# Optimization experiments

Measured on AMD Instinct MI355X. Metric: run time of the kernel, lower is better.

## Reference

```python
import jax, jax.numpy as jnp
import numpy as np

B, T, C = 4, 2048, 1024


def setup_inputs() -> dict:
    key = jax.random.key(0)
    ks = jax.random.split(key, 5)
    s = 1.0 / np.sqrt(C)
    return {
        "X": jax.random.normal(ks[0], (B, T, C), dtype=jnp.float32),
        "Wq": jax.random.normal(ks[1], (C, C), dtype=jnp.float32) * s,
        "Wk": jax.random.normal(ks[2], (C, C), dtype=jnp.float32) * s,
        "Wv": jax.random.normal(ks[3], (C, C), dtype=jnp.float32) * s,
        "Wo": jax.random.normal(ks[4], (C, C), dtype=jnp.float32) * s,
    }


def reference(X, Wq, Wk, Wv, Wo):
    Bx, Tx, Cx = X.shape
    Q = X @ Wq  # [B,T,C]
    K = X @ Wk
    V = X @ Wv
    scores = jnp.einsum('btc,bsc->bts', Q, K) / jnp.sqrt(jnp.asarray(Cx, X.dtype))
    # causal mask: position t attends to s <= t
    causal = jnp.tril(jnp.ones((Tx, Tx), dtype=bool))
    scores = jnp.where(causal, scores, jnp.asarray(-jnp.inf, scores.dtype))
    weights = jax.nn.softmax(scores, axis=-1)
    out = jnp.einsum('bts,bsc->btc', weights, V)
    return out @ Wo
```

## Files before the change

kernel.cpp:

```cpp
#include <hip/hip_runtime.h>
#include <hip/hip_bf16.h>
#include <cmath>


typedef __attribute__((ext_vector_type(8))) __bf16 bf16x8;
typedef __attribute__((ext_vector_type(8))) short short8;
typedef __attribute__((ext_vector_type(4))) float f32x4;

__device__ __forceinline__ unsigned short f2bf(float f) {
  union { float f; unsigned u; } v; v.f = f;
  unsigned u = v.u;
  u += ((u >> 16) & 1u) + 0x7fffu;
  return (unsigned short)(u >> 16);
}
__device__ __forceinline__ float bf2f(unsigned short h) {
  union { unsigned u; float f; } v; v.u = ((unsigned)h) << 16;
  return v.f;
}

#define GLDS(gp, sp)                                                           \
  __builtin_amdgcn_global_load_lds(                                            \
      (const __attribute__((address_space(1))) void*)(gp),                     \
      (__attribute__((address_space(3))) void*)(sp), 16, 0, 0)

__global__ void prep(const float* __restrict__ X,
                     const float* __restrict__ w0, const float* __restrict__ w1,
                     const float* __restrict__ w2, const float* __restrict__ w3,
                     unsigned short* __restrict__ Xb,
                     unsigned short* __restrict__ wcat,
                     unsigned short* __restrict__ wvb,
                     unsigned short* __restrict__ wot,
                     int n) {
  if (blockIdx.z == 2) {
    int bx = blockIdx.x * 32, by = blockIdx.y * 32;
    int tx = threadIdx.x, ty = threadIdx.y;
#pragma unroll
    for (int i = 0; i < 32; i += 8) {
      size_t idx = (size_t)(by + ty + i) * n + bx + tx;
      wvb[idx] = f2bf(w2[idx]);
    }
  } else if (blockIdx.z < 4) {
    const float* src = blockIdx.z == 0 ? w0 : blockIdx.z == 1 ? w1 : w3;
    unsigned short* dst = blockIdx.z == 0 ? wcat
                          : blockIdx.z == 1 ? wcat + (size_t)n * n : wot;
    __shared__ float tile[32][33];
    int bx = blockIdx.x * 32, by = blockIdx.y * 32;
    int tx = threadIdx.x, ty = threadIdx.y;
#pragma unroll
    for (int i = 0; i < 32; i += 8)
      tile[ty + i][tx] = src[(size_t)(by + ty + i) * n + bx + tx];
    __syncthreads();
#pragma unroll
    for (int i = 0; i < 32; i += 8)
      dst[(size_t)(bx + ty + i) * n + by + tx] = f2bf(tile[tx][ty + i]);
  } else {
    const int bid = (blockIdx.z - 4) * 1024 + blockIdx.y * 32 + blockIdx.x;
    const int t = threadIdx.y * 32 + threadIdx.x;
    const int i = (bid * 256 + t) * 4;
    float4 f = *(const float4*)(X + i);
    ushort4 o = make_ushort4(f2bf(f.x), f2bf(f.y), f2bf(f.z), f2bf(f.w));
    *(ushort4*)(Xb + i) = o;
  }
}

template <typename OutT, int NW>
__global__ __launch_bounds__(NW * 64, NW / 2)
void gemm_bt(const unsigned short* __restrict__ A, int lda, long long sA,
             const unsigned short* __restrict__ B, int ldb, long long sB,
             OutT* __restrict__ Cp, int ldc, long long sC,
             int K, float alpha, int tri, int kcap, int gx) {
  A  += (long long)blockIdx.z * sA;
  B  += (long long)blockIdx.z * sB;
  Cp += (long long)blockIdx.z * sC;

  int by, bx;
  if (tri) {
    const int idx = blockIdx.x;
    by = (int)((sqrtf(8.f * idx + 1.f) - 1.f) * 0.5f);
    while (by * (by + 1) / 2 > idx) --by;
    while ((by + 1) * (by + 2) / 2 <= idx) ++by;
    bx = idx - by * (by + 1) / 2;
  } else if (gx > 0) {
    const int id = blockIdx.x;
    const int gs = gx * 8;
    const int g = id / gs, r = id - g * gs;
    bx = r >> 3;
    by = g * 8 + (r & 7);
    if (kcap) by = (gridDim.x / gx) - 1 - by;
  } else {
    by = blockIdx.y;
    bx = blockIdx.x;
  }
  const int m0 = by * 128;
  const int n0 = bx * 128;
  const int Keff = kcap ? min(K, m0 + 128) : K;

  const int tid  = threadIdx.x;
  const int lane = tid & 63;
  const int w    = tid >> 6;
  const int wm   = (NW == 4) ? (w >> 1) * 64 : (w >> 1) * 32;
  const int wn   = (w & 1) * 64;
  const int quad = lane >> 4;
  const int l16  = lane & 15;
  constexpr int AI = (NW == 4) ? 4 : 2;
  constexpr int NR = 128 / (NW * 8);

  __shared__ unsigned short As[8192];
  __shared__ unsigned short Bs[8192];

  f32x4 acc[AI][4];
#pragma unroll
  for (int i = 0; i < AI; ++i)
#pragma unroll
    for (int j = 0; j < 4; ++j)
      acc[i][j] = (f32x4){0.f, 0.f, 0.f, 0.f};

  const int srow = tid >> 3;
  const int scol = ((tid & 7) ^ (srow & 7)) * 8;
  const unsigned short* gA = A + (long long)(m0 + srow) * lda + scol;
  const unsigned short* gB = B + (long long)(n0 + srow) * ldb + scol;
  const int rsw = l16 & 7;

  for (int kt = 0; kt < Keff; kt += 64) {
    __syncthreads();
#pragma unroll
    for (int r = 0; r < NR; ++r) {
      GLDS(gA + (long long)(r * NW * 8) * lda + kt, As + r * NW * 512 + tid * 8);
      GLDS(gB + (long long)(r * NW * 8) * ldb + kt, Bs + r * NW * 512 + tid * 8);
    }
    __syncthreads();
#pragma unroll
    for (int ks = 0; ks < 2; ++ks) {
      bf16x8 af[AI], bfr[4];
#pragma unroll
      for (int i = 0; i < AI; ++i)
        af[i] = *(const bf16x8*)(As + (wm + i * 16 + l16) * 64 +
                                 ((ks * 4 + quad) ^ rsw) * 8);
#pragma unroll
      for (int j = 0; j < 4; ++j)
        bfr[j] = *(const bf16x8*)(Bs + (wn + j * 16 + l16) * 64 +
                                  ((ks * 4 + quad) ^ rsw) * 8);
#pragma unroll
      for (int i = 0; i < AI; ++i)
#pragma unroll
        for (int j = 0; j < 4; ++j)
          acc[i][j] = __builtin_amdgcn_mfma_f32_16x16x32_bf16(af[i], bfr[j],
                                                              acc[i][j], 0, 0, 0);
    }
  }

#pragma unroll
  for (int i = 0; i < AI; ++i) {
#pragma unroll
    for (int j = 0; j < 4; ++j) {
      const int row = m0 + wm + i * 16 + quad * 4;
      const int col = n0 + wn + j * 16 + l16;
#pragma unroll
      for (int r = 0; r < 4; ++r) {
        float v = acc[i][j][r] * alpha;
        if constexpr (sizeof(OutT) == 2)
          Cp[(long long)(row + r) * ldc + col] = (OutT)f2bf(v);
        else
          Cp[(long long)(row + r) * ldc + col] = v;
      }
    }
  }
}


#define STG(tt, st, bb) do {                                                  \
    const int ld_ = (st) < 2 ? lda : ldb;                                     \
    const unsigned short* gp_ = ((st) < 2 ? gA : gB)                          \
        + (long long)(((st) & 1) * 128) * ld_ + (long long)(tt) * 64;         \
    unsigned short* sp_ = smem + ((bb) << 15) + (((st) >= 2) ? 16384 : 0)     \
        + (((st) & 1) * 128) * 64 + tid * 8;                                  \
    GLDS(gp_, sp_);                                                           \
    GLDS(gp_ + (long long)64 * ld_, sp_ + 4096);                              \
  } while (0)

#define LDA_PH(mh)                                                            \
  _Pragma("unroll") for (int i = 0; i < 4; ++i)                               \
  _Pragma("unroll") for (int ks = 0; ks < 2; ++ks)                            \
    bA[i][ks] = *(const bf16x8*)(Ab + (wm + (mh) * 64 + i * 16 + l16) * 64 +  \
                                 (((ks * 4 + quad) ^ rsw) * 8));

#define LDB_PH(j0)                                                            \
  _Pragma("unroll") for (int j = 0; j < 2; ++j)                               \
  _Pragma("unroll") for (int ks = 0; ks < 2; ++ks)                            \
    bB[(j0) + j][ks] = *(const bf16x8*)(Bb + (wn + ((j0) + j) * 16 + l16) * 64\
                                        + (((ks * 4 + quad) ^ rsw) * 8));

#define MM(mh, j0)                                                            \
  _Pragma("unroll") for (int i = 0; i < 4; ++i)                               \
  _Pragma("unroll") for (int j = 0; j < 2; ++j)                               \
  _Pragma("unroll") for (int ks = 0; ks < 2; ++ks)                            \
    acc[(mh) * 4 + i][(j0) + j] = __builtin_amdgcn_mfma_f32_16x16x32_bf16(    \
        bA[i][ks], bB[(j0) + j][ks], acc[(mh) * 4 + i][(j0) + j], 0, 0, 0);

#define PHASE_SYNC()                                                          \
  __builtin_amdgcn_s_barrier();                                               \
  asm volatile("s_waitcnt lgkmcnt(0)" ::: "memory");                          \
  __builtin_amdgcn_sched_barrier(0);

#define GROUP(T_, B_) do {                                                    \
    const unsigned short* Ab = smem + ((B_) << 15);                           \
    const unsigned short* Bb = Ab + 16384;                                    \
                                                                      \
    LDA_PH(0); LDB_PH(0);                                                     \
    if ((T_) + 1 < nt) STG((T_) + 1, 1, (B_) ^ 1);                            \
    asm volatile("s_waitcnt lgkmcnt(8)" ::: "memory");                        \
    PHASE_SYNC();                                                             \
    __builtin_amdgcn_s_setprio(1); MM(0, 0); __builtin_amdgcn_s_setprio(0);   \
    __builtin_amdgcn_s_barrier();                                             \
                                                                      \
    LDB_PH(2);                                                                \
    if ((T_) + 1 < nt) STG((T_) + 1, 2, (B_) ^ 1);                            \
    PHASE_SYNC();                                                             \
    __builtin_amdgcn_s_setprio(1); MM(0, 2); __builtin_amdgcn_s_setprio(0);   \
    __builtin_amdgcn_s_barrier();                                             \
                                                                      \
    LDA_PH(1);                                                                \
    if ((T_) + 1 < nt) STG((T_) + 1, 3, (B_) ^ 1);                            \
    PHASE_SYNC();                                                             \
    __builtin_amdgcn_s_setprio(1); MM(1, 2); __builtin_amdgcn_s_setprio(0);   \
    __builtin_amdgcn_s_barrier();                                             \
                                                                      \
    if ((T_) + 2 < nt) {                                                      \
      STG((T_) + 2, 0, (B_));                                                 \
      asm volatile("s_waitcnt vmcnt(2)" ::: "memory");                        \
    } else {                                                                  \
      asm volatile("s_waitcnt vmcnt(0)" ::: "memory");                        \
    }                                                                         \
    __builtin_amdgcn_s_barrier();                                             \
    __builtin_amdgcn_s_setprio(1); MM(1, 0); __builtin_amdgcn_s_setprio(0);   \
    __builtin_amdgcn_s_barrier();                                             \
  } while (0)

__global__ __launch_bounds__(512, 2)
void gemm_qkv8(const unsigned short* __restrict__ A, int lda,
               const unsigned short* __restrict__ B, int ldb,
               unsigned short* __restrict__ Cp, int K) {
  const int id  = blockIdx.x;
  const int cpx = gridDim.x >> 3;
  const int sw  = (id & 7) * cpx + (id >> 3);
  const int bx  = sw % 12;
  const int by  = sw / 12;
  const int m0  = by * 256;
  const int n0  = bx * 256;

  const int tid  = threadIdx.x;
  const int lane = tid & 63;
  const int w    = tid >> 6;
  const int wm   = (w >> 2) * 128;
  const int wn   = (w & 3) * 64;
  const int quad = lane >> 4;
  const int l16  = lane & 15;
  const int rsw  = l16 & 7;

  extern __shared__ unsigned short smem[];

  const int srow = tid >> 3;
  const int scol = ((tid & 7) ^ (srow & 7)) * 8;
  const unsigned short* gA = A + (long long)(m0 + srow) * lda + scol;
  const unsigned short* gB = B + (long long)(n0 + srow) * ldb + scol;

  f32x4 acc[8][4];
#pragma unroll
  for (int i = 0; i < 8; ++i)
#pragma unroll
    for (int j = 0; j < 4; ++j)
      acc[i][j] = (f32x4){0.f, 0.f, 0.f, 0.f};

  bf16x8 bA[4][2], bB[4][2];
  const int nt = K >> 6;

  STG(0, 0, 0); STG(0, 1, 0); STG(0, 2, 0); STG(0, 3, 0);
  STG(1, 0, 1);
  asm volatile("s_waitcnt vmcnt(2)" ::: "memory");
  __builtin_amdgcn_s_barrier();

  for (int tt = 0; tt < nt; tt += 2) {
    GROUP(tt, 0);
    GROUP(tt + 1, 1);
  }

#pragma unroll
  for (int i = 0; i < 8; ++i) {
#pragma unroll
    for (int j = 0; j < 4; ++j) {
      const int row = m0 + wm + i * 16 + quad * 4;
      const int col = n0 + wn + j * 16 + l16;
      if (col >= 2048) {
        const int b = row >> 11, t = row & 2047, cv = col - 2048;
        ushort4 o = make_ushort4(f2bf(acc[i][j][0]), f2bf(acc[i][j][1]),
                                 f2bf(acc[i][j][2]), f2bf(acc[i][j][3]));
        *(ushort4*)(Cp + 16777216LL + ((long long)(b * 1024 + cv)) * 2048 + t) = o;
      } else {
        unsigned short* dst = Cp + (col >= 1024 ? 8388608LL - 1024 : 0);
#pragma unroll
        for (int r2 = 0; r2 < 4; ++r2)
          dst[(long long)(row + r2) * 1024 + col] = f2bf(acc[i][j][r2]);
      }
    }
  }
}

#undef GROUP
#undef PHASE_SYNC
#undef MM
#undef LDB_PH
#undef LDA_PH
#undef STG

__global__ __launch_bounds__(256)
void softmax_causal(const unsigned short* __restrict__ Sin,
                    unsigned short* __restrict__ Sout, int T) {
  const long long row = blockIdx.x;
  const int t = (int)(row & (long long)(T - 1));
  const int limit = ((t >> 7) + 1) << 7;
  const unsigned short* pin = Sin + row * T;
  unsigned short* pout = Sout + row * T;
  const int tid  = threadIdx.x;
  const int base = tid * 8;
  const bool active = base < limit;

  short8 raw = {};
  if (active) raw = *(const short8*)(pin + base);
  float x[8];
  float mx = -1e30f;
#pragma unroll
  for (int j = 0; j < 8; ++j) {
    bool valid = active && (base + j) <= t;
    x[j] = valid ? bf2f((unsigned short)raw[j]) : -1e30f;
    mx = fmaxf(mx, x[j]);
  }
#pragma unroll
  for (int off = 32; off > 0; off >>= 1) mx = fmaxf(mx, __shfl_xor(mx, off));
  __shared__ float red[8];
  const int wv = tid >> 6;
  if ((tid & 63) == 0) red[wv] = mx;
  __syncthreads();
  mx = fmaxf(fmaxf(red[0], red[1]), fmaxf(red[2], red[3]));

  float sum = 0.f;
#pragma unroll
  for (int j = 0; j < 8; ++j) {
    bool valid = active && (base + j) <= t;
    x[j] = valid ? __expf(x[j] - mx) : 0.f;
    sum += x[j];
  }
#pragma unroll
  for (int off = 32; off > 0; off >>= 1) sum += __shfl_xor(sum, off);
  if ((tid & 63) == 0) red[4 + wv] = sum;
  __syncthreads();
  sum = red[4] + red[5] + red[6] + red[7];
  const float inv = 1.f / sum;

  if (active) {
    unsigned short out[8];
#pragma unroll
    for (int j = 0; j < 8; ++j) out[j] = f2bf(x[j] * inv);
    *(short8*)(pout + base) = *(const short8*)out;
  }
}

extern "C" void kernel_launch(void* const* d_in, const int* in_sizes, int n_in,
                              void* d_out, int out_size, void* d_ws,
                              size_t ws_size, hipStream_t stream) {
  (void)in_sizes; (void)n_in; (void)out_size; (void)ws_size;
  const int Bb = 4, T = 2048, C = 1024;
  const int M = Bb * T;

  const float* X  = (const float*)d_in[0];
  const float* Wq = (const float*)d_in[1];
  const float* Wk = (const float*)d_in[2];
  const float* Wv = (const float*)d_in[3];
  const float* Wo = (const float*)d_in[4];

  char* w = (char*)d_ws;
  unsigned short* Wcat = (unsigned short*)w; w += (size_t)3 * C * C * 2;
  unsigned short* Q    = (unsigned short*)w; w += (size_t)M * C * 2;
  unsigned short* Kb   = (unsigned short*)w; w += (size_t)M * C * 2;
  unsigned short* Vt   = (unsigned short*)w; w += (size_t)M * C * 2;
  unsigned short* Xb   = (unsigned short*)w; w += (size_t)M * C * 2;
  (void)Kb;
  unsigned short* Wvb  = (unsigned short*)d_out;
  unsigned short* Wot  = (unsigned short*)d_out + (size_t)C * C;
  unsigned short* S    = (unsigned short*)d_out;
  unsigned short* Sn   = Q;

  static int smem_set = 0;
  if (!smem_set) {
    hipFuncSetAttribute(reinterpret_cast<const void*>(gemm_qkv8),
                        hipFuncAttributeMaxDynamicSharedMemorySize, 131072);
    smem_set = 1;
  }

  prep<<<dim3(32, 32, 12), dim3(32, 8), 0, stream>>>(X, Wq, Wk, Wv, Wo, Xb,
                                                     Wcat, Wvb, Wot, C);

  gemm_bt<unsigned short, 4><<<dim3(C / 128, C / 128, 1), dim3(256), 0, stream>>>(
      Wot, C, 0, Wvb, C, 0, Wcat + (size_t)2 * C * C, C, 0, C, 1.f, 0, 0, 0);

  gemm_qkv8<<<dim3((M / 256) * (3 * C / 256)), dim3(512), 131072, stream>>>(
      Xb, C, Wcat, C, Q, C);

  const int ntri = (T / 128) * (T / 128 + 1) / 2;
  gemm_bt<unsigned short, 8><<<dim3(ntri, 1, Bb), dim3(512), 0, stream>>>(
      Q, C, (long long)T * C, Kb, C, (long long)T * C,
      S, T, (long long)T * T, C, 0.03125f, 1, 0, 0);

  softmax_causal<<<M, 256, 0, stream>>>(S, Sn, T);

  gemm_bt<float, 8><<<dim3((C / 128) * (T / 128), 1, Bb), dim3(512), 0, stream>>>(
      Sn, T, (long long)T * T, Vt, T, (long long)C * T,
      (float*)d_out, C, (long long)T * C, T, 1.f, 0, 1, C / 128);
}
```

Measured before the change: 269.0 us.

## Reassign QKV GEMM warp tiles to quadrants and deepen global-to-LDS prefetch pipeline

Each warp's tile in the fused QKV GEMM now spans strided 64x32 slices across the four 128x128 quadrants of the block tile, instead of one contiguous 128x64 region. Each phase's LDS reads therefore cover a block-wide quadrant. The staging order of global-to-LDS loads is rearranged, and the vmcnt waits are loosened from 2 to 6 outstanding loads, with a peeled epilogue for the last two k-tiles. The aim is more overlap between global loads and MFMA work. In exchange, the wait counts and phase ordering get more intricate and are easy to get wrong.

```diff
diff --git a/kernel.cpp b/kernel.cpp
--- a/kernel.cpp
+++ b/kernel.cpp
@@ -181,58 +181,52 @@
 #define LDA_PH(mh)                                                            \
   _Pragma("unroll") for (int i = 0; i < 4; ++i)                               \
   _Pragma("unroll") for (int ks = 0; ks < 2; ++ks)                            \
-    bA[i][ks] = *(const bf16x8*)(Ab + (wm + (mh) * 64 + i * 16 + l16) * 64 +  \
-                                 (((ks * 4 + quad) ^ rsw) * 8));
-
-#define LDB_PH(j0)                                                            \
-  _Pragma("unroll") for (int j = 0; j < 2; ++j)                               \
+    bA[i][ks] = *(const bf16x8*)(Ab + ((mh) * 128 + wm64 + i * 16 + l16) * 64 \
+                                 + (((ks * 4 + quad) ^ rsw) * 8));
+
+#define LDB_PH(jh)                                                            \
+  _Pragma("unroll") for (int jj = 0; jj < 2; ++jj)                            \
   _Pragma("unroll") for (int ks = 0; ks < 2; ++ks)                            \
-    bB[(j0) + j][ks] = *(const bf16x8*)(Bb + (wn + ((j0) + j) * 16 + l16) * 64\
-                                        + (((ks * 4 + quad) ^ rsw) * 8));
-
-#define MM(mh, j0)                                                            \
+    bB[(jh) * 2 + jj][ks] = *(const bf16x8*)(                                 \
+        Bb + ((jh) * 128 + wn32 + jj * 16 + l16) * 64 +                       \
+        (((ks * 4 + quad) ^ rsw) * 8));
+
+#define MM(mh, jh)                                                            \
   _Pragma("unroll") for (int i = 0; i < 4; ++i)                               \
-  _Pragma("unroll") for (int j = 0; j < 2; ++j)                               \
+  _Pragma("unroll") for (int jj = 0; jj < 2; ++jj)                            \
   _Pragma("unroll") for (int ks = 0; ks < 2; ++ks)                            \
-    acc[(mh) * 4 + i][(j0) + j] = __builtin_amdgcn_mfma_f32_16x16x32_bf16(    \
-        bA[i][ks], bB[(j0) + j][ks], acc[(mh) * 4 + i][(j0) + j], 0, 0, 0);
+    acc[(mh) * 4 + i][(jh) * 2 + jj] =                                        \
+        __builtin_amdgcn_mfma_f32_16x16x32_bf16(                              \
+            bA[i][ks], bB[(jh) * 2 + jj][ks],                                 \
+            acc[(mh) * 4 + i][(jh) * 2 + jj], 0, 0, 0);
+
+#define VMCNT(n) asm volatile("s_waitcnt vmcnt(" #n ")" ::: "memory")
+#define SP1 __builtin_amdgcn_s_setprio(1)
+#define SP0 __builtin_amdgcn_s_setprio(0)
 
 #define PHASE_SYNC()                                                          \
   __builtin_amdgcn_s_barrier();                                               \
   asm volatile("s_waitcnt lgkmcnt(0)" ::: "memory");                          \
   __builtin_amdgcn_sched_barrier(0);
 
-#define GROUP(T_, B_) do {                                                    \
+#define GROUP(B_, S1, S2, S3, S4, W1, W2, W4) do {                            \
     const unsigned short* Ab = smem + ((B_) << 15);                           \
     const unsigned short* Bb = Ab + 16384;                                    \
-                                                                      \
-    LDA_PH(0); LDB_PH(0);                                                     \
-    if ((T_) + 1 < nt) STG((T_) + 1, 1, (B_) ^ 1);                            \
-    asm volatile("s_waitcnt lgkmcnt(8)" ::: "memory");                        \
-    PHASE_SYNC();                                                             \
-    __builtin_amdgcn_s_setprio(1); MM(0, 0); __builtin_amdgcn_s_setprio(0);   \
+                                                   \
+    LDA_PH(0); LDB_PH(0); S1; W1; PHASE_SYNC();                               \
+    SP1; MM(0, 0); SP0;                                                       \
     __builtin_amdgcn_s_barrier();                                             \
-                                                                      \
-    LDB_PH(2);                                                                \
-    if ((T_) + 1 < nt) STG((T_) + 1, 2, (B_) ^ 1);                            \
-    PHASE_SYNC();                                                             \
-    __builtin_amdgcn_s_setprio(1); MM(0, 2); __builtin_amdgcn_s_setprio(0);   \
+                                                          \
+    LDB_PH(1); S2; W2; PHASE_SYNC();                                          \
+    SP1; MM(0, 1); SP0;                                                       \
     __builtin_amdgcn_s_barrier();                                             \
-                                                                      \
-    LDA_PH(1);                                                                \
-    if ((T_) + 1 < nt) STG((T_) + 1, 3, (B_) ^ 1);                            \
-    PHASE_SYNC();                                                             \
-    __builtin_amdgcn_s_setprio(1); MM(1, 2); __builtin_amdgcn_s_setprio(0);   \
+                                                          \
+    LDA_PH(1); S3; PHASE_SYNC();                                              \
+    SP1; MM(1, 1); SP0;                                                       \
     __builtin_amdgcn_s_barrier();                                             \
-                                                                      \
-    if ((T_) + 2 < nt) {                                                      \
-      STG((T_) + 2, 0, (B_));                                                 \
-      asm volatile("s_waitcnt vmcnt(2)" ::: "memory");                        \
-    } else {                                                                  \
-      asm volatile("s_waitcnt vmcnt(0)" ::: "memory");                        \
-    }                                                                         \
-    __builtin_amdgcn_s_barrier();                                             \
-    __builtin_amdgcn_s_setprio(1); MM(1, 0); __builtin_amdgcn_s_setprio(0);   \
+                                                            \
+    S4; W4; PHASE_SYNC();                                                     \
+    SP1; MM(1, 0); SP0;                                                       \
     __builtin_amdgcn_s_barrier();                                             \
   } while (0)
 
@@ -251,8 +245,8 @@
   const int tid  = threadIdx.x;
   const int lane = tid & 63;
   const int w    = tid >> 6;
-  const int wm   = (w >> 2) * 128;
-  const int wn   = (w & 3) * 64;
+  const int wm64 = (w >> 2) * 64;
+  const int wn32 = (w & 3) * 32;
   const int quad = lane >> 4;
   const int l16  = lane & 15;
   const int rsw  = l16 & 7;
@@ -274,32 +268,37 @@
   bf16x8 bA[4][2], bB[4][2];
   const int nt = K >> 6;
 
-  STG(0, 0, 0); STG(0, 1, 0); STG(0, 2, 0); STG(0, 3, 0);
+  STG(0, 0, 0); STG(0, 2, 0); STG(0, 3, 0); STG(0, 1, 0);
   STG(1, 0, 1);
-  asm volatile("s_waitcnt vmcnt(2)" ::: "memory");
+  VMCNT(6);
   __builtin_amdgcn_s_barrier();
 
-  for (int tt = 0; tt < nt; tt += 2) {
-    GROUP(tt, 0);
-    GROUP(tt + 1, 1);
-  }
-
-#pragma unroll
-  for (int i = 0; i < 8; ++i) {
-#pragma unroll
-    for (int j = 0; j < 4; ++j) {
-      const int row = m0 + wm + i * 16 + quad * 4;
-      const int col = n0 + wn + j * 16 + l16;
+  for (int tt = 0; tt < nt - 2; tt += 2) {
+    GROUP(0, STG(tt + 1, 2, 1), STG(tt + 1, 3, 1), STG(tt + 1, 1, 1),
+          STG(tt + 2, 0, 0), VMCNT(6), VMCNT(6), VMCNT(6));
+    GROUP(1, STG(tt + 2, 2, 0), STG(tt + 2, 3, 0), STG(tt + 2, 1, 0),
+          STG(tt + 3, 0, 1), VMCNT(6), VMCNT(6), VMCNT(6));
+  }
+  GROUP(0, STG(nt - 1, 2, 1), STG(nt - 1, 3, 1), STG(nt - 1, 1, 1),
+        (void)0, VMCNT(6), VMCNT(6), VMCNT(4));
+  GROUP(1, (void)0, (void)0, (void)0, (void)0, VMCNT(2), VMCNT(0), (void)0);
+
+#pragma unroll
+  for (int mi = 0; mi < 8; ++mi) {
+#pragma unroll
+    for (int nj = 0; nj < 4; ++nj) {
+      const int row = m0 + (mi >> 2) * 128 + wm64 + (mi & 3) * 16 + quad * 4;
+      const int col = n0 + (nj >> 1) * 128 + wn32 + (nj & 1) * 16 + l16;
       if (col >= 2048) {
         const int b = row >> 11, t = row & 2047, cv = col - 2048;
-        ushort4 o = make_ushort4(f2bf(acc[i][j][0]), f2bf(acc[i][j][1]),
-                                 f2bf(acc[i][j][2]), f2bf(acc[i][j][3]));
+        ushort4 o = make_ushort4(f2bf(acc[mi][nj][0]), f2bf(acc[mi][nj][1]),
+                                 f2bf(acc[mi][nj][2]), f2bf(acc[mi][nj][3]));
         *(ushort4*)(Cp + 16777216LL + ((long long)(b * 1024 + cv)) * 2048 + t) = o;
       } else {
         unsigned short* dst = Cp + (col >= 1024 ? 8388608LL - 1024 : 0);
 #pragma unroll
         for (int r2 = 0; r2 < 4; ++r2)
-          dst[(long long)(row + r2) * 1024 + col] = f2bf(acc[i][j][r2]);
+          dst[(long long)(row + r2) * 1024 + col] = f2bf(acc[mi][nj][r2]);
       }
     }
   }
@@ -307,6 +306,9 @@
 
 #undef GROUP
 #undef PHASE_SYNC
+#undef SP1
+#undef SP0
+#undef VMCNT
 #undef MM
 #undef LDB_PH
 #undef LDA_PH
```

After: 264.7 us. About the same (-1.6%).
